# Optimization experiments

Hardware: AMD Instinct MI355X
Metric: run time of the kernel (lower is better)

Reference implementation:

```python
import jax, jax.numpy as jnp
import numpy as np

N_USERS = 50000
N_ITEMS = 150000
N = N_USERS + N_ITEMS
N_EDGES = 1250000
D = 64
N_LAYERS = 3


def setup_inputs() -> dict:
    key = jax.random.key(0)
    ks = jax.random.split(key, 7)
    edge_src = jax.random.randint(ks[0], (N_EDGES,), 0, N, dtype=jnp.int32)
    edge_dst = jax.random.randint(ks[1], (N_EDGES,), 0, N, dtype=jnp.int32)
    edge_weight = jax.random.uniform(ks[2], (N_EDGES,), dtype=jnp.float32)
    user_emb = jax.random.normal(ks[3], (N_USERS, D), dtype=jnp.float32) * 0.1
    item_emb = jax.random.normal(ks[4], (N_ITEMS, D), dtype=jnp.float32) * 0.1
    # Ws[layer, which_linear] with which_linear in {0: W1 (on L@e), 1: W2 (on (L@e)*e), 2: W3 (on e)}
    Ws = jax.random.normal(ks[5], (N_LAYERS, 3, D, D), dtype=jnp.float32) * (1.0 / np.sqrt(D))
    bs = jnp.zeros((N_LAYERS, 3, D), dtype=jnp.float32)
    return {"edge_src": edge_src, "edge_dst": edge_dst, "edge_weight": edge_weight,
            "user_emb": user_emb, "item_emb": item_emb, "Ws": Ws, "bs": bs}


def _l2_normalize(x):
    # torch.nn.functional.normalize(p=2, dim=1, eps=1e-12)
    n = jnp.sqrt(jnp.sum(x * x, axis=1, keepdims=True))
    return x / jnp.maximum(n, 1e-12)


def reference(edge_src, edge_dst, edge_weight, user_emb, item_emb, Ws, bs):
    e = jnp.concatenate([user_emb, item_emb], axis=0)  # [N, D]
    all_embs = [e]
    for i in range(N_LAYERS):
        # SpMM: term1 = L @ e (COO scatter-add)
        term1 = jax.ops.segment_sum(edge_weight[:, None] * e[edge_src], edge_dst,
                                    num_segments=N)  # [N, D]
        term2 = term1 * e
        inter = (term1 @ Ws[i, 0] + bs[i, 0]
                 + term2 @ Ws[i, 1] + bs[i, 1]
                 + e @ Ws[i, 2] + bs[i, 2])
        inter = jax.nn.leaky_relu(inter, negative_slope=0.01)
        e = _l2_normalize(inter)  # dropout is identity in eval mode
        all_embs.append(e)
    all_embs = jnp.concatenate(all_embs, axis=1)  # [N, 4*D]
    return all_embs[:N_USERS], all_embs[N_USERS:]
```

## Files before the change

kernel.cpp:

```cpp
#include <hip/hip_runtime.h>
#include <hip/hip_bf16.h>

#define NU 50000
#define NI 150000
#define NN 200000
#define NE 1250000
#define DD 64
#define NLAYERS 3
#define SCAN_B 1024
#define NB ((NN + SCAN_B - 1) / SCAN_B)
#define BT_STRIDE 232

typedef __attribute__((ext_vector_type(8))) short bf16x8;
typedef __attribute__((ext_vector_type(4))) float f32x4;

static __device__ __forceinline__ unsigned short f2b(float x) {
  __hip_bfloat16 h = __float2bfloat16(x);
  return *reinterpret_cast<unsigned short*>(&h);
}

static __device__ __forceinline__ unsigned int pack2(float lo, float hi) {
  return (unsigned int)f2b(lo) | ((unsigned int)f2b(hi) << 16);
}

static __device__ __forceinline__ float blo(unsigned int u) { return __uint_as_float(u << 16); }
static __device__ __forceinline__ float bhi(unsigned int u) { return __uint_as_float(u & 0xffff0000u); }

static __device__ __forceinline__ bf16x8 mulbf8(bf16x8 a, bf16x8 b) {
  union { bf16x8 v; unsigned int u[4]; } A, B, R;
  A.v = a; B.v = b;
#pragma unroll
  for (int i = 0; i < 4; ++i) {
    R.u[i] = pack2(blo(A.u[i]) * blo(B.u[i]), bhi(A.u[i]) * bhi(B.u[i]));
  }
  return R.v;
}

__global__ __launch_bounds__(256) void k_zero(int* __restrict__ p) {
  int i = blockIdx.x * 256 + threadIdx.x;
  if (i < NN) p[i] = 0;
}

__global__ __launch_bounds__(256) void k_wprep(const float* __restrict__ Ws,
                                               unsigned short* __restrict__ WtBf) {
  int t = blockIdx.x * 256 + threadIdx.x;
  if (t >= 3 * 64 * 192) return;
  int j = t % 192;
  int n = (t / 192) & 63;
  int lyr = t / (192 * 64);
  WtBf[t] = f2b(Ws[((size_t)lyr * 3 + (j >> 6)) * 4096 + (size_t)(j & 63) * 64 + n]);
}

__global__ __launch_bounds__(256) void k_init(const float4* __restrict__ ue,
                                              const float4* __restrict__ ie,
                                              float4* __restrict__ out4,
                                              uint2* __restrict__ ebf2) {
  int gid = blockIdx.x * 256 + threadIdx.x;
  if (gid >= NN * 16) return;
  int row = gid >> 4, q = gid & 15;
  float4 v = (row < NU) ? ue[(size_t)row * 16 + q] : ie[(size_t)(row - NU) * 16 + q];
  out4[(size_t)row * 64 + q] = v;
  uint2 b; b.x = pack2(v.x, v.y); b.y = pack2(v.z, v.w);
  ebf2[(size_t)row * 16 + q] = b;
}

__global__ __launch_bounds__(256) void k_hist(const int* __restrict__ dst, int* __restrict__ cnt) {
  int e = blockIdx.x * 256 + threadIdx.x;
  if (e < NE) atomicAdd(&cnt[dst[e]], 1);
}

__global__ __launch_bounds__(SCAN_B) void k_scan1(const int* __restrict__ cnt,
                                                  int* __restrict__ local,
                                                  int* __restrict__ btot) {
  __shared__ int sm[SCAN_B];
  int t = threadIdx.x;
  int i = blockIdx.x * SCAN_B + t;
  int v = (i < NN) ? cnt[i] : 0;
  sm[t] = v;
  __syncthreads();
  for (int off = 1; off < SCAN_B; off <<= 1) {
    int x = (t >= off) ? sm[t - off] : 0;
    __syncthreads();
    sm[t] += x;
    __syncthreads();
  }
  if (i < NN) local[i] = sm[t] - v;
  if (t == SCAN_B - 1) btot[blockIdx.x] = sm[t];
}

__global__ __launch_bounds__(256) void k_scan2(int* __restrict__ btot) {
  __shared__ int sm[256];
  int t = threadIdx.x;
  int v = (t < NB) ? btot[t] : 0;
  sm[t] = v;
  __syncthreads();
  for (int off = 1; off < 256; off <<= 1) {
    int x = (t >= off) ? sm[t - off] : 0;
    __syncthreads();
    sm[t] += x;
    __syncthreads();
  }
  if (t < NB) btot[t] = sm[t] - v;
}

__global__ __launch_bounds__(256) void k_finalize(const int* __restrict__ local,
                                                  const int* __restrict__ btot,
                                                  int* __restrict__ row_start,
                                                  int* __restrict__ cursor) {
  int i = blockIdx.x * 256 + threadIdx.x;
  if (i < NN) {
    int v = local[i] + btot[i / SCAN_B];
    row_start[i] = v;
    cursor[i] = v;
  }
  if (i == 0) row_start[NN] = NE;
}

__global__ __launch_bounds__(256) void k_fill(const int* __restrict__ src,
                                              const int* __restrict__ dst,
                                              const float* __restrict__ w,
                                              int* __restrict__ cursor,
                                              int2* __restrict__ csr_pack) {
  int e = blockIdx.x * 256 + threadIdx.x;
  if (e < NE) {
    int p = atomicAdd(&cursor[dst[e]], 1);
    int2 pk; pk.x = src[e]; pk.y = __float_as_int(w[e]);
    csr_pack[p] = pk;
  }
}

__global__ __launch_bounds__(256) void k_spmm(const int* __restrict__ row_start,
                                              const int2* __restrict__ csr_pack,
                                              const unsigned int* __restrict__ ebf,
                                              unsigned int* __restrict__ t1bf) {
  int gid = blockIdx.x * 256 + threadIdx.x;
  int row = gid >> 6;
  if (row >= NN) return;
  const int l = gid & 63;
  const int eidx = l >> 3;
  const int cb = l & 7;
  int s0 = row_start[row];
  int s1 = row_start[row + 1];

  float a0 = 0.f, a1 = 0.f, a2 = 0.f, a3 = 0.f, a4 = 0.f, a5 = 0.f, a6 = 0.f, a7 = 0.f;

  if (s0 < s1) {
    int j0 = s0 + eidx, j1 = s0 + 8 + eidx;
    int2 p0 = csr_pack[j0 < s1 ? j0 : 0];
    int2 p1 = csr_pack[j1 < s1 ? j1 : 0];
    uint4 v0 = *reinterpret_cast<const uint4*>(ebf + (size_t)p0.x * 32 + cb * 4);
    uint4 v1 = *reinterpret_cast<const uint4*>(ebf + (size_t)p1.x * 32 + cb * 4);
    float w0 = (j0 < s1) ? __int_as_float(p0.y) : 0.f;
    float w1 = (j1 < s1) ? __int_as_float(p1.y) : 0.f;
    a0 = fmaf(w0, blo(v0.x), a0); a1 = fmaf(w0, bhi(v0.x), a1);
    a2 = fmaf(w0, blo(v0.y), a2); a3 = fmaf(w0, bhi(v0.y), a3);
    a4 = fmaf(w0, blo(v0.z), a4); a5 = fmaf(w0, bhi(v0.z), a5);
    a6 = fmaf(w0, blo(v0.w), a6); a7 = fmaf(w0, bhi(v0.w), a7);
    a0 = fmaf(w1, blo(v1.x), a0); a1 = fmaf(w1, bhi(v1.x), a1);
    a2 = fmaf(w1, blo(v1.y), a2); a3 = fmaf(w1, bhi(v1.y), a3);
    a4 = fmaf(w1, blo(v1.z), a4); a5 = fmaf(w1, bhi(v1.z), a5);
    a6 = fmaf(w1, blo(v1.w), a6); a7 = fmaf(w1, bhi(v1.w), a7);
    for (int base = s0 + 16; base < s1; base += 8) {
      int j = base + eidx;
      int2 p = csr_pack[j < s1 ? j : 0];
      uint4 v = *reinterpret_cast<const uint4*>(ebf + (size_t)p.x * 32 + cb * 4);
      float wt = (j < s1) ? __int_as_float(p.y) : 0.f;
      a0 = fmaf(wt, blo(v.x), a0); a1 = fmaf(wt, bhi(v.x), a1);
      a2 = fmaf(wt, blo(v.y), a2); a3 = fmaf(wt, bhi(v.y), a3);
      a4 = fmaf(wt, blo(v.z), a4); a5 = fmaf(wt, bhi(v.z), a5);
      a6 = fmaf(wt, blo(v.w), a6); a7 = fmaf(wt, bhi(v.w), a7);
    }
  }

  a0 += __shfl_xor(a0, 8, 64);  a0 += __shfl_xor(a0, 16, 64);  a0 += __shfl_xor(a0, 32, 64);
  a1 += __shfl_xor(a1, 8, 64);  a1 += __shfl_xor(a1, 16, 64);  a1 += __shfl_xor(a1, 32, 64);
  a2 += __shfl_xor(a2, 8, 64);  a2 += __shfl_xor(a2, 16, 64);  a2 += __shfl_xor(a2, 32, 64);
  a3 += __shfl_xor(a3, 8, 64);  a3 += __shfl_xor(a3, 16, 64);  a3 += __shfl_xor(a3, 32, 64);
  a4 += __shfl_xor(a4, 8, 64);  a4 += __shfl_xor(a4, 16, 64);  a4 += __shfl_xor(a4, 32, 64);
  a5 += __shfl_xor(a5, 8, 64);  a5 += __shfl_xor(a5, 16, 64);  a5 += __shfl_xor(a5, 32, 64);
  a6 += __shfl_xor(a6, 8, 64);  a6 += __shfl_xor(a6, 16, 64);  a6 += __shfl_xor(a6, 32, 64);
  a7 += __shfl_xor(a7, 8, 64);  a7 += __shfl_xor(a7, 16, 64);  a7 += __shfl_xor(a7, 32, 64);

  if (l < 8) {
    uint4 st;
    st.x = pack2(a0, a1); st.y = pack2(a2, a3); st.z = pack2(a4, a5); st.w = pack2(a6, a7);
    *reinterpret_cast<uint4*>(t1bf + (size_t)row * 32 + l * 4) = st;
  }
}

__global__ __launch_bounds__(256) void k_row_mfma(const unsigned int* __restrict__ t1bf,
                                                  const unsigned int* __restrict__ ebf,
                                                  const unsigned short* __restrict__ WtBf,
                                                  const float* __restrict__ bs,
                                                  float* __restrict__ out,
                                                  unsigned short* __restrict__ ebf_next,
                                                  int layer, int wbf) {
  __shared__ unsigned short Bt[64][BT_STRIDE];
  const int tid = threadIdx.x;
  {
    const uint4* __restrict__ src = reinterpret_cast<const uint4*>(WtBf + (size_t)layer * 64 * 192);
#pragma unroll
    for (int ch = tid; ch < 1536; ch += 256) {
      int rown = ch / 24, k = ch % 24;
      *reinterpret_cast<uint4*>(&Bt[rown][k * 8]) = src[ch];
    }
  }
  __syncthreads();

  const int l = tid & 63;
  const int wv = tid >> 6;
  const int g = l >> 4;
  const int li = l & 15;
  const int rowbase = blockIdx.x * 64 + wv * 16;
  const int r = rowbase + li;

  const unsigned short* __restrict__ t1b = reinterpret_cast<const unsigned short*>(t1bf);
  const unsigned short* __restrict__ eb = reinterpret_cast<const unsigned short*>(ebf);
  bf16x8 A0 = *reinterpret_cast<const bf16x8*>(t1b + (size_t)r * 64 + 8 * g);
  bf16x8 A1 = *reinterpret_cast<const bf16x8*>(t1b + (size_t)r * 64 + 32 + 8 * g);
  bf16x8 E0 = *reinterpret_cast<const bf16x8*>(eb + (size_t)r * 64 + 8 * g);
  bf16x8 E1 = *reinterpret_cast<const bf16x8*>(eb + (size_t)r * 64 + 32 + 8 * g);
  bf16x8 T0 = mulbf8(A0, E0);
  bf16x8 T1 = mulbf8(A1, E1);

  const float* __restrict__ bsl = bs + (size_t)layer * 3 * 64;
  f32x4 acc[4];
#pragma unroll
  for (int f = 0; f < 4; ++f) {
    int n = f * 16 + li;
    float bv = bsl[n] + bsl[64 + n] + bsl[128 + n];
    acc[f] = (f32x4){bv, bv, bv, bv};
  }

  bf16x8 Afr[6] = {A0, A1, T0, T1, E0, E1};
#pragma unroll
  for (int s = 0; s < 6; ++s) {
#pragma unroll
    for (int f = 0; f < 4; ++f) {
      const bf16x8 Bf = *reinterpret_cast<const bf16x8*>(&Bt[f * 16 + li][s * 32 + 8 * g]);
      acc[f] = __builtin_amdgcn_mfma_f32_16x16x32_bf16(Afr[s], Bf, acc[f], 0, 0, 0);
    }
  }

  float p[4];
#pragma unroll
  for (int reg = 0; reg < 4; ++reg) {
    float ssum = 0.f;
#pragma unroll
    for (int f = 0; f < 4; ++f) {
      float x = acc[f][reg];
      x = (x >= 0.f) ? x : 0.01f * x;
      acc[f][reg] = x;
      ssum = fmaf(x, x, ssum);
    }
    p[reg] = ssum;
  }
#pragma unroll
  for (int off = 1; off < 16; off <<= 1) {
#pragma unroll
    for (int reg = 0; reg < 4; ++reg) p[reg] += __shfl_xor(p[reg], off, 64);
  }
  float inv[4];
#pragma unroll
  for (int reg = 0; reg < 4; ++reg) inv[reg] = 1.0f / fmaxf(sqrtf(p[reg]), 1e-12f);

  float* __restrict__ ob = out + (size_t)(layer + 1) * 64;
#pragma unroll
  for (int reg = 0; reg < 4; ++reg) {
#pragma unroll
    for (int f = 0; f < 4; ++f) {
      float val = acc[f][reg] * inv[reg];
      ob[(size_t)(rowbase + 4 * g + reg) * 256 + f * 16 + li] = val;
      if (wbf) ebf_next[(size_t)(rowbase + 4 * g + reg) * 64 + f * 16 + li] = f2b(val);
    }
  }
}

extern "C" void kernel_launch(void* const* d_in, const int* in_sizes, int n_in,
                              void* d_out, int out_size, void* d_ws, size_t ws_size,
                              hipStream_t stream) {
  const int* edge_src = (const int*)d_in[0];
  const int* edge_dst = (const int*)d_in[1];
  const float* edge_w = (const float*)d_in[2];
  const float* user_emb = (const float*)d_in[3];
  const float* item_emb = (const float*)d_in[4];
  const float* Ws = (const float*)d_in[5];
  const float* bs = (const float*)d_in[6];
  float* out = (float*)d_out;

  char* w = (char*)d_ws;
  unsigned int* ebfA = (unsigned int*)w; w += (size_t)NN * 32 * 4;
  unsigned int* ebfB = (unsigned int*)w; w += (size_t)NN * 32 * 4;
  unsigned int* t1bf = (unsigned int*)w; w += (size_t)NN * 32 * 4;
  int2* csr_pack = (int2*)w;      w += (size_t)NE * 8;
  unsigned short* WtBf = (unsigned short*)w; w += (size_t)3 * 64 * 192 * 2;
  int* cnt = (int*)w;             w += (size_t)NN * 4;
  int* local = (int*)w;           w += (size_t)NN * 4;
  int* row_start = (int*)w;       w += (size_t)(NN + 4) * 4;
  int* cursor = (int*)w;          w += (size_t)NN * 4;
  int* btot = (int*)w;            w += 256 * 4;

  k_zero<<<(NN + 255) / 256, 256, 0, stream>>>(cnt);
  k_wprep<<<(3 * 64 * 192 + 255) / 256, 256, 0, stream>>>(Ws, WtBf);
  k_init<<<(NN * 16 + 255) / 256, 256, 0, stream>>>(
      (const float4*)user_emb, (const float4*)item_emb, (float4*)out, (uint2*)ebfA);
  k_hist<<<(NE + 255) / 256, 256, 0, stream>>>(edge_dst, cnt);
  k_scan1<<<NB, SCAN_B, 0, stream>>>(cnt, local, btot);
  k_scan2<<<1, 256, 0, stream>>>(btot);
  k_finalize<<<(NN + 255) / 256, 256, 0, stream>>>(local, btot, row_start, cursor);
  k_fill<<<(NE + 255) / 256, 256, 0, stream>>>(edge_src, edge_dst, edge_w, cursor, csr_pack);

  k_spmm<<<(NN * 64 + 255) / 256, 256, 0, stream>>>(row_start, csr_pack, ebfA, t1bf);
  k_row_mfma<<<NN / 64, 256, 0, stream>>>(t1bf, ebfA, WtBf, bs, out, (unsigned short*)ebfB, 0, 1);
  k_spmm<<<(NN * 64 + 255) / 256, 256, 0, stream>>>(row_start, csr_pack, ebfB, t1bf);
  k_row_mfma<<<NN / 64, 256, 0, stream>>>(t1bf, ebfB, WtBf, bs, out, (unsigned short*)ebfA, 1, 1);
  k_spmm<<<(NN * 64 + 255) / 256, 256, 0, stream>>>(row_start, csr_pack, ebfA, t1bf);
  k_row_mfma<<<NN / 64, 256, 0, stream>>>(t1bf, ebfA, WtBf, bs, out, (unsigned short*)ebfB, 2, 0);
}
```

Baseline: 411.0 us.

## Fuse setup kernels, add low-degree SpMM path, enlarge MFMA blocks

Merges the zeroing, weight-prep and embedding-init kernels into one setup launch to cut launch overhead. The SpMM now skips the second gather batch when a row has at most eight edges, and clamps out-of-range indices to the row's last edge instead of index 0, to avoid wasted gathers. The row MFMA kernel now uses 512-thread blocks covering 128 rows, with a guard for the partial final block. The risks are more divergence in the SpMM branch and an early return in partially filled MFMA blocks.

```diff
diff --git a/kernel.cpp b/kernel.cpp
--- a/kernel.cpp
+++ b/kernel.cpp
@@ -36,32 +36,28 @@
   return R.v;
 }
 
-__global__ __launch_bounds__(256) void k_zero(int* __restrict__ p) {
-  int i = blockIdx.x * 256 + threadIdx.x;
-  if (i < NN) p[i] = 0;
-}
-
-__global__ __launch_bounds__(256) void k_wprep(const float* __restrict__ Ws,
-                                               unsigned short* __restrict__ WtBf) {
-  int t = blockIdx.x * 256 + threadIdx.x;
-  if (t >= 3 * 64 * 192) return;
-  int j = t % 192;
-  int n = (t / 192) & 63;
-  int lyr = t / (192 * 64);
-  WtBf[t] = f2b(Ws[((size_t)lyr * 3 + (j >> 6)) * 4096 + (size_t)(j & 63) * 64 + n]);
-}
-
-__global__ __launch_bounds__(256) void k_init(const float4* __restrict__ ue,
-                                              const float4* __restrict__ ie,
-                                              float4* __restrict__ out4,
-                                              uint2* __restrict__ ebf2) {
+__global__ __launch_bounds__(256) void k_setup(const float4* __restrict__ ue,
+                                               const float4* __restrict__ ie,
+                                               float4* __restrict__ out4,
+                                               uint2* __restrict__ ebf2,
+                                               const float* __restrict__ Ws,
+                                               unsigned short* __restrict__ WtBf,
+                                               int* __restrict__ cnt) {
   int gid = blockIdx.x * 256 + threadIdx.x;
-  if (gid >= NN * 16) return;
-  int row = gid >> 4, q = gid & 15;
-  float4 v = (row < NU) ? ue[(size_t)row * 16 + q] : ie[(size_t)(row - NU) * 16 + q];
-  out4[(size_t)row * 64 + q] = v;
-  uint2 b; b.x = pack2(v.x, v.y); b.y = pack2(v.z, v.w);
-  ebf2[(size_t)row * 16 + q] = b;
+  if (gid < NN * 16) {
+    int row = gid >> 4, q = gid & 15;
+    float4 v = (row < NU) ? ue[(size_t)row * 16 + q] : ie[(size_t)(row - NU) * 16 + q];
+    out4[(size_t)row * 64 + q] = v;
+    uint2 b; b.x = pack2(v.x, v.y); b.y = pack2(v.z, v.w);
+    ebf2[(size_t)row * 16 + q] = b;
+  }
+  if (gid < NN) cnt[gid] = 0;
+  if (gid < 3 * 64 * 192) {
+    int j = gid % 192;
+    int n = (gid / 192) & 63;
+    int lyr = gid / (192 * 64);
+    WtBf[gid] = f2b(Ws[((size_t)lyr * 3 + (j >> 6)) * 4096 + (size_t)(j & 63) * 64 + n]);
+  }
 }
 
 __global__ __launch_bounds__(256) void k_hist(const int* __restrict__ dst, int* __restrict__ cnt) {
@@ -141,34 +137,49 @@
   const int cb = l & 7;
   int s0 = row_start[row];
   int s1 = row_start[row + 1];
+  int deg = s1 - s0;
 
   float a0 = 0.f, a1 = 0.f, a2 = 0.f, a3 = 0.f, a4 = 0.f, a5 = 0.f, a6 = 0.f, a7 = 0.f;
 
-  if (s0 < s1) {
-    int j0 = s0 + eidx, j1 = s0 + 8 + eidx;
-    int2 p0 = csr_pack[j0 < s1 ? j0 : 0];
-    int2 p1 = csr_pack[j1 < s1 ? j1 : 0];
+  if (deg > 0) {
+    int j0 = s0 + eidx;
+    bool e0 = j0 < s1;
+    j0 = e0 ? j0 : s1 - 1;
+    int2 p0 = csr_pack[j0];
     uint4 v0 = *reinterpret_cast<const uint4*>(ebf + (size_t)p0.x * 32 + cb * 4);
-    uint4 v1 = *reinterpret_cast<const uint4*>(ebf + (size_t)p1.x * 32 + cb * 4);
-    float w0 = (j0 < s1) ? __int_as_float(p0.y) : 0.f;
-    float w1 = (j1 < s1) ? __int_as_float(p1.y) : 0.f;
-    a0 = fmaf(w0, blo(v0.x), a0); a1 = fmaf(w0, bhi(v0.x), a1);
-    a2 = fmaf(w0, blo(v0.y), a2); a3 = fmaf(w0, bhi(v0.y), a3);
-    a4 = fmaf(w0, blo(v0.z), a4); a5 = fmaf(w0, bhi(v0.z), a5);
-    a6 = fmaf(w0, blo(v0.w), a6); a7 = fmaf(w0, bhi(v0.w), a7);
-    a0 = fmaf(w1, blo(v1.x), a0); a1 = fmaf(w1, bhi(v1.x), a1);
-    a2 = fmaf(w1, blo(v1.y), a2); a3 = fmaf(w1, bhi(v1.y), a3);
-    a4 = fmaf(w1, blo(v1.z), a4); a5 = fmaf(w1, bhi(v1.z), a5);
-    a6 = fmaf(w1, blo(v1.w), a6); a7 = fmaf(w1, bhi(v1.w), a7);
-    for (int base = s0 + 16; base < s1; base += 8) {
-      int j = base + eidx;
-      int2 p = csr_pack[j < s1 ? j : 0];
-      uint4 v = *reinterpret_cast<const uint4*>(ebf + (size_t)p.x * 32 + cb * 4);
-      float wt = (j < s1) ? __int_as_float(p.y) : 0.f;
-      a0 = fmaf(wt, blo(v.x), a0); a1 = fmaf(wt, bhi(v.x), a1);
-      a2 = fmaf(wt, blo(v.y), a2); a3 = fmaf(wt, bhi(v.y), a3);
-      a4 = fmaf(wt, blo(v.z), a4); a5 = fmaf(wt, bhi(v.z), a5);
-      a6 = fmaf(wt, blo(v.w), a6); a7 = fmaf(wt, bhi(v.w), a7);
+    float w0 = e0 ? __int_as_float(p0.y) : 0.f;
+    if (deg > 8) {
+      int j1 = s0 + 8 + eidx;
+      bool e1 = j1 < s1;
+      j1 = e1 ? j1 : s1 - 1;
+      int2 p1 = csr_pack[j1];
+      uint4 v1 = *reinterpret_cast<const uint4*>(ebf + (size_t)p1.x * 32 + cb * 4);
+      float w1 = e1 ? __int_as_float(p1.y) : 0.f;
+      a0 = fmaf(w0, blo(v0.x), a0); a1 = fmaf(w0, bhi(v0.x), a1);
+      a2 = fmaf(w0, blo(v0.y), a2); a3 = fmaf(w0, bhi(v0.y), a3);
+      a4 = fmaf(w0, blo(v0.z), a4); a5 = fmaf(w0, bhi(v0.z), a5);
+      a6 = fmaf(w0, blo(v0.w), a6); a7 = fmaf(w0, bhi(v0.w), a7);
+      a0 = fmaf(w1, blo(v1.x), a0); a1 = fmaf(w1, bhi(v1.x), a1);
+      a2 = fmaf(w1, blo(v1.y), a2); a3 = fmaf(w1, bhi(v1.y), a3);
+      a4 = fmaf(w1, blo(v1.z), a4); a5 = fmaf(w1, bhi(v1.z), a5);
+      a6 = fmaf(w1, blo(v1.w), a6); a7 = fmaf(w1, bhi(v1.w), a7);
+      for (int base = s0 + 16; base < s1; base += 8) {
+        int j = base + eidx;
+        bool ev = j < s1;
+        j = ev ? j : s1 - 1;
+        int2 p = csr_pack[j];
+        uint4 v = *reinterpret_cast<const uint4*>(ebf + (size_t)p.x * 32 + cb * 4);
+        float wt = ev ? __int_as_float(p.y) : 0.f;
+        a0 = fmaf(wt, blo(v.x), a0); a1 = fmaf(wt, bhi(v.x), a1);
+        a2 = fmaf(wt, blo(v.y), a2); a3 = fmaf(wt, bhi(v.y), a3);
+        a4 = fmaf(wt, blo(v.z), a4); a5 = fmaf(wt, bhi(v.z), a5);
+        a6 = fmaf(wt, blo(v.w), a6); a7 = fmaf(wt, bhi(v.w), a7);
+      }
+    } else {
+      a0 = fmaf(w0, blo(v0.x), a0); a1 = fmaf(w0, bhi(v0.x), a1);
+      a2 = fmaf(w0, blo(v0.y), a2); a3 = fmaf(w0, bhi(v0.y), a3);
+      a4 = fmaf(w0, blo(v0.z), a4); a5 = fmaf(w0, bhi(v0.z), a5);
+      a6 = fmaf(w0, blo(v0.w), a6); a7 = fmaf(w0, bhi(v0.w), a7);
     }
   }
 
@@ -188,7 +199,7 @@
   }
 }
 
-__global__ __launch_bounds__(256) void k_row_mfma(const unsigned int* __restrict__ t1bf,
+__global__ __launch_bounds__(512) void k_row_mfma(const unsigned int* __restrict__ t1bf,
                                                   const unsigned int* __restrict__ ebf,
                                                   const unsigned short* __restrict__ WtBf,
                                                   const float* __restrict__ bs,
@@ -200,7 +211,7 @@
   {
     const uint4* __restrict__ src = reinterpret_cast<const uint4*>(WtBf + (size_t)layer * 64 * 192);
 #pragma unroll
-    for (int ch = tid; ch < 1536; ch += 256) {
+    for (int ch = tid; ch < 1536; ch += 512) {
       int rown = ch / 24, k = ch % 24;
       *reinterpret_cast<uint4*>(&Bt[rown][k * 8]) = src[ch];
     }
@@ -211,7 +222,8 @@
   const int wv = tid >> 6;
   const int g = l >> 4;
   const int li = l & 15;
-  const int rowbase = blockIdx.x * 64 + wv * 16;
+  const int rowbase = blockIdx.x * 128 + wv * 16;
+  if (rowbase >= NN) return;
   const int r = rowbase + li;
 
   const unsigned short* __restrict__ t1b = reinterpret_cast<const unsigned short*>(t1bf);
@@ -300,10 +312,9 @@
   int* cursor = (int*)w;          w += (size_t)NN * 4;
   int* btot = (int*)w;            w += 256 * 4;
 
-  k_zero<<<(NN + 255) / 256, 256, 0, stream>>>(cnt);
-  k_wprep<<<(3 * 64 * 192 + 255) / 256, 256, 0, stream>>>(Ws, WtBf);
-  k_init<<<(NN * 16 + 255) / 256, 256, 0, stream>>>(
-      (const float4*)user_emb, (const float4*)item_emb, (float4*)out, (uint2*)ebfA);
+  k_setup<<<(NN * 16 + 255) / 256, 256, 0, stream>>>(
+      (const float4*)user_emb, (const float4*)item_emb, (float4*)out, (uint2*)ebfA,
+      Ws, WtBf, cnt);
   k_hist<<<(NE + 255) / 256, 256, 0, stream>>>(edge_dst, cnt);
   k_scan1<<<NB, SCAN_B, 0, stream>>>(cnt, local, btot);
   k_scan2<<<1, 256, 0, stream>>>(btot);
@@ -311,9 +322,9 @@
   k_fill<<<(NE + 255) / 256, 256, 0, stream>>>(edge_src, edge_dst, edge_w, cursor, csr_pack);
 
   k_spmm<<<(NN * 64 + 255) / 256, 256, 0, stream>>>(row_start, csr_pack, ebfA, t1bf);
-  k_row_mfma<<<NN / 64, 256, 0, stream>>>(t1bf, ebfA, WtBf, bs, out, (unsigned short*)ebfB, 0, 1);
+  k_row_mfma<<<(NN + 127) / 128, 512, 0, stream>>>(t1bf, ebfA, WtBf, bs, out, (unsigned short*)ebfB, 0, 1);
   k_spmm<<<(NN * 64 + 255) / 256, 256, 0, stream>>>(row_start, csr_pack, ebfB, t1bf);
-  k_row_mfma<<<NN / 64, 256, 0, stream>>>(t1bf, ebfB, WtBf, bs, out, (unsigned short*)ebfA, 1, 1);
+  k_row_mfma<<<(NN + 127) / 128, 512, 0, stream>>>(t1bf, ebfB, WtBf, bs, out, (unsigned short*)ebfA, 1, 1);
   k_spmm<<<(NN * 64 + 255) / 256, 256, 0, stream>>>(row_start, csr_pack, ebfA, t1bf);
-  k_row_mfma<<<NN / 64, 256, 0, stream>>>(t1bf, ebfA, WtBf, bs, out, (unsigned short*)ebfB, 2, 0);
-}
+  k_row_mfma<<<(NN + 127) / 128, 512, 0, stream>>>(t1bf, ebfA, WtBf, bs, out, (unsigned short*)ebfB, 2, 0);
+}
```

Result: no change. 412.6 us (+0.4%).
